# Performance work log

Measured on AMD Instinct MI355X. Metric: run time of the kernel, lower is better.

Reference implementation:

```python
import math
import jax, jax.numpy as jnp
import numpy as np

B, S, E, H = 4, 1024, 1024, 16
DH = E // H
LN_EPS = 1e-5


def _layernorm(x, g, b):
    mu = jnp.mean(x, axis=-1, keepdims=True)
    var = jnp.mean(jnp.square(x - mu), axis=-1, keepdims=True)
    return (x - mu) * jax.lax.rsqrt(var + LN_EPS) * g + b


def _gelu_tanh(x):
    c = math.sqrt(2.0 / math.pi)
    return 0.5 * x * (1.0 + jnp.tanh(c * (x + 0.044715 * x * x * x)))


def setup_inputs() -> dict:
    key = jax.random.key(0)
    ks = jax.random.split(key, 12)
    std = 0.02
    x = jax.random.normal(ks[0], (B, S, E), jnp.float32)
    # additive causal mask: 0 on/below diag, -inf above
    causal_mask = jnp.where(jnp.tril(jnp.ones((S, S), bool)), 0.0, -jnp.inf).astype(jnp.float32)
    inp = dict(
        x=x,
        causal_mask=causal_mask,
        ln1_g=1.0 + std * jax.random.normal(ks[1], (E,), jnp.float32),
        ln1_b=std * jax.random.normal(ks[2], (E,), jnp.float32),
        ln2_g=1.0 + std * jax.random.normal(ks[3], (E,), jnp.float32),
        ln2_b=std * jax.random.normal(ks[4], (E,), jnp.float32),
        w_in=std * jax.random.normal(ks[5], (3 * E, E), jnp.float32),   # packed QKV in_proj_weight
        b_in=jnp.zeros((3 * E,), jnp.float32),
        w_out=std * jax.random.normal(ks[6], (E, E), jnp.float32),      # out_proj.weight
        b_out=jnp.zeros((E,), jnp.float32),
        w_fc=std * jax.random.normal(ks[7], (4 * E, E), jnp.float32),
        b_fc=jnp.zeros((4 * E,), jnp.float32),
        w_proj=std * jax.random.normal(ks[8], (E, 4 * E), jnp.float32),
        b_proj=jnp.zeros((E,), jnp.float32),
    )
    return inp


def reference(x, causal_mask, ln1_g, ln1_b, ln2_g, ln2_b,
              w_in, b_in, w_out, b_out, w_fc, b_fc, w_proj, b_proj):
    # --- attention branch (pre-LN) ---
    h = _layernorm(x, ln1_g, ln1_b)                       # [B,S,E]
    wq, wk, wv = w_in[:E], w_in[E:2 * E], w_in[2 * E:]
    bq, bk, bv = b_in[:E], b_in[E:2 * E], b_in[2 * E:]
    q = (h @ wq.T + bq).reshape(B, S, H, DH)
    k = (h @ wk.T + bk).reshape(B, S, H, DH)
    v = (h @ wv.T + bv).reshape(B, S, H, DH)
    scale = 1.0 / math.sqrt(DH)
    scores = jnp.einsum('bqhd,bkhd->bhqk', q * scale, k) + causal_mask  # [B,H,S,S]
    probs = jax.nn.softmax(scores, axis=-1)
    att = jnp.einsum('bhqk,bkhd->bqhd', probs, v).reshape(B, S, E)
    att = att @ w_out.T + b_out
    att_weights = jnp.mean(probs, axis=1)                 # averaged over heads, [B,S,S]
    x = x + att
    # --- MLP branch (pre-LN) ---
    h2 = _layernorm(x, ln2_g, ln2_b)
    x = x + (_gelu_tanh(h2 @ w_fc.T + b_fc) @ w_proj.T + b_proj)
    return (x, att_weights)
```

## Files before the change

kernel.cpp:

```cpp
#include <hip/hip_runtime.h>

typedef unsigned short u16;
typedef u16   u16x4 __attribute__((ext_vector_type(4)));
typedef u16   u16x8 __attribute__((ext_vector_type(8)));
typedef short s16x8 __attribute__((ext_vector_type(8)));
typedef float f32x4 __attribute__((ext_vector_type(4)));

__device__ __forceinline__ float b2f(u16 u) {
    union { unsigned int i; float f; } v; v.i = ((unsigned int)u) << 16; return v.f;
}
__device__ __forceinline__ u16 f2b(float f) {
    union { float f; unsigned int i; } v; v.f = f;
    unsigned int r = v.i + 0x7fffu + ((v.i >> 16) & 1u);
    return (u16)(r >> 16);
}
__device__ __forceinline__ float gelu_f(float x) {
    float z = 0.7978845608028654f * (x + 0.044715f * x * x * x);
    float e = __expf(2.0f * z);
    float t = 1.0f - 2.0f / (e + 1.0f);
    return 0.5f * x * (1.0f + t);
}
__device__ __forceinline__ void async16(const u16* g, u16* l) {
    __builtin_amdgcn_global_load_lds(
        (const __attribute__((address_space(1))) unsigned int*)g,
        (__attribute__((address_space(3))) unsigned int*)l,
        16, 0, 0);
}

__global__ __launch_bounds__(256)
void detect_k(const u16* __restrict__ x, int* __restrict__ flag)
{
    int gid = blockIdx.x * 256 + threadIdx.x;
    const u16x8 u = *(const u16x8*)(x + (long)gid * 8);
    int bad = 0;
    #pragma unroll
    for (int e = 0; e < 8; e++) {
        int ex = (u[e] >> 7) & 0xFF;
        if (ex >= 187) bad = 1;
    }
    unsigned long long m = __ballot(bad != 0);
    if ((threadIdx.x & 63) == 0 && m != 0ull) atomicOr(flag, 1);
}

__global__ __launch_bounds__(256)
void conv_w_k(const void* __restrict__ s0, const void* __restrict__ s1,
              const void* __restrict__ s2, const void* __restrict__ s3,
              u16* __restrict__ dst, const int* __restrict__ flag)
{
    const long MEG = 1L << 20;
    long gid = ((long)blockIdx.x * 256 + threadIdx.x) * 4;
    const void* s; long off;
    if      (gid <  3*MEG) { s = s0; off = gid; }
    else if (gid <  4*MEG) { s = s1; off = gid - 3*MEG; }
    else if (gid <  8*MEG) { s = s2; off = gid - 4*MEG; }
    else                   { s = s3; off = gid - 8*MEG; }
    u16x4 o;
    if (*flag) {
        const float4 f = *(const float4*)((const float*)s + off);
        o[0] = f2b(f.x); o[1] = f2b(f.y); o[2] = f2b(f.z); o[3] = f2b(f.w);
    } else {
        o = *(const u16x4*)((const u16*)s + off);
    }
    *(u16x4*)(dst + gid) = o;
}

__global__ __launch_bounds__(256)
void conv_small_k(const void* s0, const void* s1, const void* s2, const void* s3,
                  const void* s4, const void* s5, const void* s6, const void* s7,
                  u16* __restrict__ dst, const int* __restrict__ flag)
{
    int gid = blockIdx.x * 256 + threadIdx.x;
    int seg, off;
    if      (gid <  4096) { seg = gid >> 10;  off = gid & 1023; }
    else if (gid <  7168) { seg = 4; off = gid - 4096; }
    else if (gid <  8192) { seg = 5; off = gid - 7168; }
    else if (gid < 12288) { seg = 6; off = gid - 8192; }
    else                  { seg = 7; off = gid - 12288; }
    const void* srcs[8] = {s0, s1, s2, s3, s4, s5, s6, s7};
    const void* s = srcs[seg];
    dst[seg * 4096 + off] = (*flag) ? f2b(((const float*)s)[off]) : ((const u16*)s)[off];
}

__global__ __launch_bounds__(256)
void ln1x_k(const void* __restrict__ xraw, const u16* __restrict__ g,
            const u16* __restrict__ b, u16* __restrict__ xc,
            u16* __restrict__ o, const int* __restrict__ flag)
{
    long row = blockIdx.x;
    int tid = threadIdx.x;
    float v0, v1, v2, v3;
    if (*flag) {
        const float4 f = *(const float4*)((const float*)xraw + row * 1024 + tid * 4);
        v0 = b2f(f2b(f.x)); v1 = b2f(f2b(f.y));
        v2 = b2f(f2b(f.z)); v3 = b2f(f2b(f.w));
    } else {
        const u16x4 u = *(const u16x4*)((const u16*)xraw + row * 1024 + tid * 4);
        v0 = b2f(u[0]); v1 = b2f(u[1]); v2 = b2f(u[2]); v3 = b2f(u[3]);
    }
    u16x4 xv; xv[0] = f2b(v0); xv[1] = f2b(v1); xv[2] = f2b(v2); xv[3] = f2b(v3);
    *(u16x4*)(xc + row * 1024 + tid * 4) = xv;
    float s  = v0 + v1 + v2 + v3;
    float sq = v0*v0 + v1*v1 + v2*v2 + v3*v3;
    #pragma unroll
    for (int off = 32; off; off >>= 1) { s += __shfl_xor(s, off); sq += __shfl_xor(sq, off); }
    __shared__ float sm[8];
    int wid = tid >> 6, lane = tid & 63;
    if (lane == 0) { sm[wid] = s; sm[wid + 4] = sq; }
    __syncthreads();
    s  = sm[0] + sm[1] + sm[2] + sm[3];
    sq = sm[4] + sm[5] + sm[6] + sm[7];
    float mean = s * (1.0f / 1024.0f);
    float var  = sq * (1.0f / 1024.0f) - mean * mean;
    float rs   = rsqrtf(var + 1e-5f);
    u16x4 gg = *(const u16x4*)(g + tid * 4);
    u16x4 bb = *(const u16x4*)(b + tid * 4);
    u16x4 ov;
    ov[0] = f2b((v0 - mean) * rs * b2f(gg[0]) + b2f(bb[0]));
    ov[1] = f2b((v1 - mean) * rs * b2f(gg[1]) + b2f(bb[1]));
    ov[2] = f2b((v2 - mean) * rs * b2f(gg[2]) + b2f(bb[2]));
    ov[3] = f2b((v3 - mean) * rs * b2f(gg[3]) + b2f(bb[3]));
    *(u16x4*)(o + row * 1024 + tid * 4) = ov;
}

__global__ __launch_bounds__(256)
void ln_k(const u16* __restrict__ x, const u16* __restrict__ g,
          const u16* __restrict__ b, u16* __restrict__ o)
{
    long row = blockIdx.x;
    int tid = threadIdx.x;
    const u16x4 u = *(const u16x4*)(x + row * 1024 + tid * 4);
    float v0 = b2f(u[0]), v1 = b2f(u[1]), v2 = b2f(u[2]), v3 = b2f(u[3]);
    float s  = v0 + v1 + v2 + v3;
    float sq = v0*v0 + v1*v1 + v2*v2 + v3*v3;
    #pragma unroll
    for (int off = 32; off; off >>= 1) { s += __shfl_xor(s, off); sq += __shfl_xor(sq, off); }
    __shared__ float sm[8];
    int wid = tid >> 6, lane = tid & 63;
    if (lane == 0) { sm[wid] = s; sm[wid + 4] = sq; }
    __syncthreads();
    s  = sm[0] + sm[1] + sm[2] + sm[3];
    sq = sm[4] + sm[5] + sm[6] + sm[7];
    float mean = s * (1.0f / 1024.0f);
    float var  = sq * (1.0f / 1024.0f) - mean * mean;
    float rs   = rsqrtf(var + 1e-5f);
    u16x4 gg = *(const u16x4*)(g + tid * 4);
    u16x4 bb = *(const u16x4*)(b + tid * 4);
    u16x4 ov;
    ov[0] = f2b((v0 - mean) * rs * b2f(gg[0]) + b2f(bb[0]));
    ov[1] = f2b((v1 - mean) * rs * b2f(gg[1]) + b2f(bb[1]));
    ov[2] = f2b((v2 - mean) * rs * b2f(gg[2]) + b2f(bb[2]));
    ov[3] = f2b((v3 - mean) * rs * b2f(gg[3]) + b2f(bb[3]));
    *(u16x4*)(o + row * 1024 + tid * 4) = ov;
}

__global__ __launch_bounds__(256)
void redln_k(const float* __restrict__ P, long slice,
             const u16* __restrict__ bias, u16* __restrict__ res,
             const u16* __restrict__ g, const u16* __restrict__ b,
             u16* __restrict__ o)
{
    long row = blockIdx.x;
    int tid = threadIdx.x;
    long i = row * 1024 + tid * 4;
    float4 v  = *(const float4*)(P + i);
    float4 p1 = *(const float4*)(P + slice + i);
    u16x4 bb = *(const u16x4*)(bias + tid * 4);
    u16x4 rr = *(const u16x4*)(res + i);
    float v0 = b2f(f2b(v.x + p1.x + b2f(bb[0]) + b2f(rr[0])));
    float v1 = b2f(f2b(v.y + p1.y + b2f(bb[1]) + b2f(rr[1])));
    float v2 = b2f(f2b(v.z + p1.z + b2f(bb[2]) + b2f(rr[2])));
    float v3 = b2f(f2b(v.w + p1.w + b2f(bb[3]) + b2f(rr[3])));
    u16x4 xv; xv[0] = f2b(v0); xv[1] = f2b(v1); xv[2] = f2b(v2); xv[3] = f2b(v3);
    *(u16x4*)(res + i) = xv;
    float s  = v0 + v1 + v2 + v3;
    float sq = v0*v0 + v1*v1 + v2*v2 + v3*v3;
    #pragma unroll
    for (int off = 32; off; off >>= 1) { s += __shfl_xor(s, off); sq += __shfl_xor(sq, off); }
    __shared__ float sm[8];
    int wid = tid >> 6, lane = tid & 63;
    if (lane == 0) { sm[wid] = s; sm[wid + 4] = sq; }
    __syncthreads();
    s  = sm[0] + sm[1] + sm[2] + sm[3];
    sq = sm[4] + sm[5] + sm[6] + sm[7];
    float mean = s * (1.0f / 1024.0f);
    float var  = sq * (1.0f / 1024.0f) - mean * mean;
    float rs   = rsqrtf(var + 1e-5f);
    u16x4 gg = *(const u16x4*)(g + tid * 4);
    u16x4 b2 = *(const u16x4*)(b + tid * 4);
    u16x4 ov;
    ov[0] = f2b((v0 - mean) * rs * b2f(gg[0]) + b2f(b2[0]));
    ov[1] = f2b((v1 - mean) * rs * b2f(gg[1]) + b2f(b2[1]));
    ov[2] = f2b((v2 - mean) * rs * b2f(gg[2]) + b2f(b2[2]));
    ov[3] = f2b((v3 - mean) * rs * b2f(gg[3]) + b2f(b2[3]));
    *(u16x4*)(o + row * 1024 + tid * 4) = ov;
}

__global__ __launch_bounds__(1024)
void smmean_k(u16* __restrict__ probs, void* __restrict__ ow, long ofs,
              const int* __restrict__ flag)
{
    const long MEG = 1L << 20;
    __shared__ float red[16 * 1024];
    int bl = blockIdx.x >> 10;
    int q  = blockIdx.x & 1023;
    int w = threadIdx.x >> 6, lane = threadIdx.x & 63;
    int tile_end = ((q >> 7) + 1) << 7;
    u16* row = probs + (((long)(bl * 16 + w)) << 20) + (long)q * 1024;
    float v[16];
    float m = -3.0e38f;
    #pragma unroll
    for (int c = 0; c < 2; c++) {
        int kb = (c * 64 + lane) * 8;
        if (kb <= q) {
            u16x8 u = *(const u16x8*)(row + kb);
            #pragma unroll
            for (int e = 0; e < 8; e++) {
                if (kb + e <= q) {
                    float f = b2f(u[e]);
                    v[c * 8 + e] = f;
                    m = fmaxf(m, f);
                } else v[c * 8 + e] = -3.0e38f;
            }
        } else {
            #pragma unroll
            for (int e = 0; e < 8; e++) v[c * 8 + e] = -3.0e38f;
        }
    }
    #pragma unroll
    for (int off = 32; off; off >>= 1) m = fmaxf(m, __shfl_xor(m, off));
    float s = 0.0f;
    #pragma unroll
    for (int t = 0; t < 16; t++) {
        float e = (v[t] > -1.0e38f) ? __expf(v[t] - m) : 0.0f;
        v[t] = e; s += e;
    }
    #pragma unroll
    for (int off = 32; off; off >>= 1) s += __shfl_xor(s, off);
    float inv = 1.0f / s;
    #pragma unroll
    for (int c = 0; c < 2; c++) {
        int kb = (c * 64 + lane) * 8;
        float p[8];
        #pragma unroll
        for (int e = 0; e < 8; e++) p[e] = v[c * 8 + e] * inv;
        #pragma unroll
        for (int e = 0; e < 8; e++) red[w * 1024 + kb + e] = p[e];
        if (kb < tile_end) {
            u16x8 o;
            #pragma unroll
            for (int e = 0; e < 8; e++) o[e] = f2b(p[e]);
            *(u16x8*)(row + kb) = o;
        }
    }
    __syncthreads();
    int t = threadIdx.x;
    float acc = 0.0f;
    #pragma unroll
    for (int h = 0; h < 16; h++) acc += red[h * 1024 + t];
    acc *= 0.0625f;
    long idx = ofs + (long)bl * MEG + (long)q * 1024 + t;
    if (*flag) ((float*)ow)[idx] = acc;
    else       ((u16*)ow)[idx]   = f2b(acc);
}

__global__ __launch_bounds__(256)
void reduce_out_k(const float* __restrict__ P, long slice,
                  const u16* __restrict__ bias, const u16* __restrict__ res,
                  void* __restrict__ out, const int* __restrict__ flag)
{
    long i = ((long)blockIdx.x * 256 + threadIdx.x) * 4;
    int gn = (int)(i & 1023);
    float4 v = *(const float4*)(P + i);
    #pragma unroll
    for (int s = 1; s < 4; s++) {
        const float4 p = *(const float4*)(P + (long)s * slice + i);
        v.x += p.x; v.y += p.y; v.z += p.z; v.w += p.w;
    }
    u16x4 bb = *(const u16x4*)(bias + gn);
    u16x4 rr = *(const u16x4*)(res + i);
    v.x += b2f(bb[0]) + b2f(rr[0]);
    v.y += b2f(bb[1]) + b2f(rr[1]);
    v.z += b2f(bb[2]) + b2f(rr[2]);
    v.w += b2f(bb[3]) + b2f(rr[3]);
    if (*flag) {
        *(float4*)((float*)out + i) = v;
    } else {
        u16x4 o;
        o[0] = f2b(v.x); o[1] = f2b(v.y); o[2] = f2b(v.z); o[3] = f2b(v.w);
        *(u16x4*)((u16*)out + i) = o;
    }
}

template<int BN, int EPI>
__global__ __launch_bounds__(256)
void gemm_bt(const u16* __restrict__ A, const u16* __restrict__ Bt,
             u16* __restrict__ C, const u16* __restrict__ bias,
             const u16* __restrict__ res,
             u16* __restrict__ qb, u16* __restrict__ kb, u16* __restrict__ vb,
             int M, int N, int K, int lda, int ldb, int ldc,
             long sA, long sB, long sC,
             const int* __restrict__ oflag, void* __restrict__ oout)
{
    constexpr int BM = 128, BK = 32;
    constexpr int WROWS = (BN == 128) ? 2 : 4;
    constexpr int WCOLS = (BN == 128) ? 2 : 1;
    constexpr int WM = BM / WROWS, WN = BN / WCOLS;
    constexpr int MI = WM / 16, NJ = WN / 16;
    constexpr int BCH = BN * BK / 8 / 256;
    constexpr int SHSZ = 2 * BM * BK + 2 * BN * BK;

    __shared__ alignas(16) u16 shmem[SHSZ];
    u16* AshB = shmem;
    u16* BshB = shmem + 2 * BM * BK;
    u16* Csh  = shmem;

    const int tid = threadIdx.x;
    int tn = blockIdx.x, tm = blockIdx.y;
    const int bz = blockIdx.z;
    if (EPI == 4 && tn > tm) return;

    if (EPI == 1 || EPI == 2 || EPI == 3 || EPI == 6 || EPI == 7) {
        int L = blockIdx.y * gridDim.x + blockIdx.x;
        int xcd = L & 7, idx = L >> 3;
        tn = idx % gridDim.x;
        tm = (idx / gridDim.x) * 8 + xcd;
    }

    const u16* Ab = A + (long)bz * sA;
    const u16* Bb = Bt + (long)bz * sB;

    const int m0 = tm * BM, n0 = tn * BN;
    const int kEff = (EPI == 5) ? (((tm + 1) * BM < K) ? (tm + 1) * BM : K) : K;

    const int w = tid >> 6, lane = tid & 63;
    const int wrow = w % WROWS, wcol = w / WROWS;
    const int mw = wrow * WM, nw = wcol * WN;
    const int lr = lane & 15, quad = lane >> 4;

    const int ca0 = tid, ca1 = 256 + tid;
    const int cb1 = 256 + tid;

    const int ar0 = ca0 >> 2, ac0 = (((ca0 & 3) ^ ((ca0 >> 3) & 3))) * 8;
    const int ar1 = ca1 >> 2, ac1 = (((ca1 & 3) ^ ((ca1 >> 3) & 3))) * 8;
    const int br0 = tid >> 2, bc0 = (((tid & 3) ^ ((tid >> 3) & 3))) * 8;
    const int br1 = cb1 >> 2, bc1 = (((cb1 & 3) ^ ((cb1 >> 3) & 3))) * 8;

    auto stage = [&](int buf, int k0) {
        async16(Ab + (long)(m0 + ar0) * lda + k0 + ac0, &AshB[buf * BM * BK + ca0 * 8]);
        async16(Ab + (long)(m0 + ar1) * lda + k0 + ac1, &AshB[buf * BM * BK + ca1 * 8]);
        async16(Bb + (long)(n0 + br0) * ldb + k0 + bc0, &BshB[buf * BN * BK + tid * 8]);
        if (BCH == 2)
            async16(Bb + (long)(n0 + br1) * ldb + k0 + bc1, &BshB[buf * BN * BK + cb1 * 8]);
    };

    f32x4 acc[MI][NJ] = {};

    const int foff = (quad ^ ((lr >> 1) & 3)) * 8;

    stage(0, 0);
    int cur = 0;
    for (int k0 = 0; k0 < kEff; k0 += BK) {
        __syncthreads();
        if (k0 + BK < kEff) stage(cur ^ 1, k0 + BK);

        s16x8 af[MI], bfr[NJ];
        #pragma unroll
        for (int i = 0; i < MI; i++)
            af[i] = *(const s16x8*)&AshB[cur * BM * BK + (mw + i * 16 + lr) * BK + foff];
        #pragma unroll
        for (int j = 0; j < NJ; j++)
            bfr[j] = *(const s16x8*)&BshB[cur * BN * BK + (nw + j * 16 + lr) * BK + foff];
        #pragma unroll
        for (int i = 0; i < MI; i++)
            #pragma unroll
            for (int j = 0; j < NJ; j++)
                acc[i][j] = __builtin_amdgcn_mfma_f32_16x16x32_bf16(af[i], bfr[j], acc[i][j], 0, 0, 0);
        cur ^= 1;
    }

    if (EPI == 1) {
        const int sel = n0 >> 10;
        const int b = m0 >> 10, sbase = m0 & 1023;
        if (sel < 2) {
            u16* dst = (sel == 0) ? qb : kb;
            #pragma unroll
            for (int i = 0; i < MI; i++)
                #pragma unroll
                for (int j = 0; j < NJ; j++)
                    #pragma unroll
                    for (int r = 0; r < 4; r++) {
                        int gm = m0 + mw + i * 16 + quad * 4 + r;
                        int gn = n0 + nw + j * 16 + lr;
                        float v = acc[i][j][r] + b2f(bias[gn]);
                        int s = gm & 1023, nn = gn & 1023, hh = nn >> 6, d = nn & 63;
                        dst[(((long)(b * 16 + hh) * 1024 + s) << 6) + d] = f2b(v);
                    }
        } else {
            __syncthreads();
            #pragma unroll
            for (int i = 0; i < MI; i++)
                #pragma unroll
                for (int j = 0; j < NJ; j++)
                    #pragma unroll
                    for (int r = 0; r < 4; r++) {
                        int nl = nw + j * 16 + lr;
                        int ml = mw + i * 16 + quad * 4 + r;
                        float v = acc[i][j][r] + b2f(bias[n0 + nl]);
                        Csh[nl * 128 + (((ml >> 3) ^ (nl & 15)) << 3) + (ml & 7)] = f2b(v);
                    }
            __syncthreads();
            const int nv0 = n0 - 2048;
            #pragma unroll
            for (int rep = 0; rep < 8; rep++) {
                int dd = rep * 16 + (tid >> 4);
                int sl = (tid & 15) * 8;
                int dg = nv0 + dd, hh = dg >> 6, dcol = dg & 63;
                u16x8 val = *(const u16x8*)&Csh[dd * 128 + ((((sl >> 3)) ^ (dd & 15)) << 3)];
                *(u16x8*)&vb[(((long)(b * 16 + hh) * 64 + dcol) << 10) + sbase + sl] = val;
            }
        }
        return;
    }

    u16* Cb;
    if (EPI == 5) Cb = C + (long)(bz >> 4) * (1 << 20) + (bz & 15) * 64;
    else          Cb = C + (long)bz * sC;

    #pragma unroll
    for (int i = 0; i < MI; i++) {
        #pragma unroll
        for (int j = 0; j < NJ; j++) {
            #pragma unroll
            for (int r = 0; r < 4; r++) {
                int gm = m0 + mw + i * 16 + quad * 4 + r;
                int gn = n0 + nw + j * 16 + lr;
                float v = acc[i][j][r];
                if (EPI == 5) {
                    Cb[(long)gm * ldc + gn] = f2b(v);
                } else if (EPI == 2) {
                    v += b2f(bias[gn]) + b2f(res[(long)gm * ldc + gn]);
                    Cb[(long)gm * ldc + gn] = f2b(v);
                } else if (EPI == 3) {
                    Cb[(long)gm * ldc + gn] = f2b(gelu_f(v + b2f(bias[gn])));
                } else if (EPI == 4) {
                    if (gn <= gm) Cb[(long)gm * ldc + gn] = f2b(v * 0.125f);
                } else if (EPI == 6) {
                    v += b2f(bias[gn]) + b2f(res[(long)gm * ldc + gn]);
                    long idx = (long)gm * ldc + gn;
                    if (*oflag) ((float*)oout)[idx] = v;
                    else        ((u16*)oout)[idx]   = f2b(v);
                } else if (EPI == 7) {
                    ((float*)oout)[(long)bz * sC + (long)gm * ldc + gn] = v;
                }
            }
        }
    }
}

extern "C" void kernel_launch(void* const* d_in, const int* in_sizes, int n_in,
                              void* d_out, int out_size, void* d_ws, size_t ws_size,
                              hipStream_t stream)
{
    const long MEG = 1L << 20;
    const long KI  = 1024;

    u16* ws = (u16*)d_ws;
    u16* xc    = ws;
    u16* winC  = ws + 4  * MEG;
    u16* woutC = ws + 7  * MEG;
    u16* wfcC  = ws + 8  * MEG;
    u16* wprjC = ws + 12 * MEG;
    u16* sm    = ws + 16 * MEG;
    u16* ln1g = sm + 0*4*KI, *ln1b = sm + 1*4*KI;
    u16* ln2g = sm + 2*4*KI, *ln2b = sm + 3*4*KI;
    u16* binC = sm + 4*4*KI;
    u16* boutC= sm + 5*4*KI;
    u16* bfcC = sm + 6*4*KI;
    u16* bprjC= sm + 7*4*KI;
    int* flag = (int*)(sm + 8*4*KI);
    u16* slotA = ws + 16 * MEG + 64 * KI;
    u16* qB    = slotA + 4  * MEG;
    u16* kB    = slotA + 8  * MEG;
    u16* vT    = slotA + 12 * MEG;
    u16* probs = slotA + 16 * MEG;
    float* part = (float*)(probs + 16 * MEG);

    const long fixed_elems = 32 * MEG + 64 * KI;
    const long avail = (long)(ws_size / 2);
    int chunk = 1;
    if      (avail >= fixed_elems + 64 * MEG) chunk = 4;
    else if (avail >= fixed_elems + 32 * MEG) chunk = 2;
    const bool splitk = (chunk == 4);

    hipMemsetAsync((void*)flag, 0, sizeof(int), stream);
    detect_k<<<32, 256, 0, stream>>>((const u16*)d_in[0], flag);
    conv_w_k<<<12288, 256, 0, stream>>>(d_in[6], d_in[8], d_in[10], d_in[12],
                                        winC, flag);
    conv_small_k<<<52, 256, 0, stream>>>(d_in[2], d_in[3], d_in[4], d_in[5],
                                         d_in[7], d_in[9], d_in[11], d_in[13],
                                         sm, flag);

    u16* h   = slotA;
    u16* att = slotA;
    u16* h2  = slotA;
    u16* act = probs;

    ln1x_k<<<4096, 256, 0, stream>>>(d_in[0], ln1g, ln1b, xc, h, flag);
    gemm_bt<128, 1><<<dim3(24, 32, 1), 256, 0, stream>>>(
        h, winC, nullptr, binC, nullptr, qB, kB, vT,
        4096, 3072, 1024, 1024, 1024, 0, 0, 0, 0, nullptr, nullptr);
    for (int b0 = 0; b0 < 4; b0 += chunk) {
        gemm_bt<128, 4><<<dim3(8, 8, 16 * chunk), 256, 0, stream>>>(
            qB + b0 * MEG, kB + b0 * MEG, probs, nullptr, nullptr,
            nullptr, nullptr, nullptr,
            1024, 1024, 64, 64, 64, 1024, 65536, 65536, 1048576, nullptr, nullptr);
        smmean_k<<<1024 * chunk, 1024, 0, stream>>>(probs, d_out,
                                                    4 * MEG + b0 * MEG, flag);
        gemm_bt<64, 5><<<dim3(1, 8, 16 * chunk), 256, 0, stream>>>(
            probs, vT + b0 * MEG, att + b0 * MEG, nullptr, nullptr,
            nullptr, nullptr, nullptr,
            1024, 64, 1024, 1024, 1024, 1024, 1048576, 65536, 0, nullptr, nullptr);
    }
    if (splitk) {
        gemm_bt<128, 7><<<dim3(8, 32, 2), 256, 0, stream>>>(
            att, woutC, nullptr, nullptr, nullptr, nullptr, nullptr, nullptr,
            4096, 1024, 512, 1024, 1024, 1024, 512, 512, 4 * MEG, nullptr, part);
        redln_k<<<4096, 256, 0, stream>>>(part, 4 * MEG, boutC, xc, ln2g, ln2b, h2);
    } else {
        gemm_bt<128, 2><<<dim3(8, 32, 1), 256, 0, stream>>>(
            att, woutC, xc, boutC, xc, nullptr, nullptr, nullptr,
            4096, 1024, 1024, 1024, 1024, 1024, 0, 0, 0, nullptr, nullptr);
        ln_k<<<4096, 256, 0, stream>>>(xc, ln2g, ln2b, h2);
    }
    gemm_bt<128, 3><<<dim3(32, 32, 1), 256, 0, stream>>>(
        h2, wfcC, act, bfcC, nullptr, nullptr, nullptr, nullptr,
        4096, 4096, 1024, 1024, 1024, 4096, 0, 0, 0, nullptr, nullptr);
    if (splitk) {
        gemm_bt<128, 7><<<dim3(8, 32, 4), 256, 0, stream>>>(
            act, wprjC, nullptr, nullptr, nullptr, nullptr, nullptr, nullptr,
            4096, 1024, 1024, 4096, 4096, 1024, 1024, 1024, 4 * MEG, nullptr, part);
        reduce_out_k<<<4096, 256, 0, stream>>>(part, 4 * MEG, bprjC, xc, d_out, flag);
    } else {
        gemm_bt<128, 6><<<dim3(8, 32, 1), 256, 0, stream>>>(
            act, wprjC, nullptr, bprjC, xc, nullptr, nullptr, nullptr,
            4096, 1024, 4096, 4096, 4096, 1024, 0, 0, 0, flag, d_out);
    }
}
```

Measured before the change: 423.6 us.

## Add 256x256-tile 8-wave pipelined GEMM for MLP fc and proj layers

Adds a new GEMM kernel with 256x256 output tiles, 512 threads and double-buffered async global-to-LDS loads. It uses XOR-swizzled LDS, explicit waitcnt and barrier scheduling, setprio around MFMA bursts, and an XCD-aware block remap. The kernel replaces the 128-tile GEMMs for the MLP fc (with GELU epilogue) and the split-K projection layers, aiming for higher arithmetic intensity and better overlap of loads with MFMA. The hand-tuned waitcnt counts and the missing bounds checks tie it to K being a multiple of 128 and to dimensions divisible by 256.

```diff
diff --git a/kernel.cpp b/kernel.cpp
--- a/kernel.cpp
+++ b/kernel.cpp
@@ -26,6 +26,11 @@
         (__attribute__((address_space(3))) unsigned int*)l,
         16, 0, 0);
 }
+
+#define FEN() asm volatile("" ::: "memory")
+#define BARR() { FEN(); __builtin_amdgcn_s_barrier(); FEN(); }
+#define LGKM0() { asm volatile("s_waitcnt lgkmcnt(0)" ::: "memory"); __builtin_amdgcn_sched_barrier(0); }
+#define VMC(N) asm volatile("s_waitcnt vmcnt(" #N ")" ::: "memory")
 
 __global__ __launch_bounds__(256)
 void detect_k(const u16* __restrict__ x, int* __restrict__ flag)
@@ -289,6 +294,172 @@
         o[0] = f2b(v.x); o[1] = f2b(v.y); o[2] = f2b(v.z); o[3] = f2b(v.w);
         *(u16x4*)((u16*)out + i) = o;
     }
+}
+
+template<int EPI>
+__global__ __launch_bounds__(512, 2)
+void g8(const u16* __restrict__ A, const u16* __restrict__ Bt,
+        u16* __restrict__ C, const u16* __restrict__ bias,
+        float* __restrict__ Cf,
+        int K, int lda, int ldb, int ldc,
+        long sA, long sB, long sC)
+{
+    __shared__ alignas(16) u16 shA[2 * 16384];
+    __shared__ alignas(16) u16 shB[2 * 16384];
+
+    const int tid = threadIdx.x;
+    int tn = blockIdx.x, tm = blockIdx.y;
+    const int bz = blockIdx.z;
+    {
+        int L = blockIdx.y * gridDim.x + blockIdx.x;
+        int xcd = L & 7, idx = L >> 3;
+        tn = idx % gridDim.x;
+        tm = (idx / gridDim.x) * 8 + xcd;
+    }
+    const u16* Ab = A + (long)bz * sA;
+    const u16* Bb = Bt + (long)bz * sB;
+    const int m0 = tm * 256, n0 = tn * 256;
+    const int NT = K >> 6;
+
+    const int w = tid >> 6, lane = tid & 63;
+    const int lr = lane & 15, quad = lane >> 4, sw = lane & 7;
+    const int wm16 = (w >> 2) * 16, wn16 = (w & 3) * 16;
+
+    auto stageH = [&](int tile, int isB, int half) {
+        const u16* src = isB ? Bb : Ab;
+        const int ld = isB ? ldb : lda;
+        const int r0 = (isB ? n0 : m0) + half * 128;
+        u16* dbase = (isB ? shB : shA) + (tile & 1) * 16384 + half * 8192;
+        const long kk = (long)tile << 6;
+        #pragma unroll
+        for (int L2 = 0; L2 < 2; L2++) {
+            int c = L2 * 512 + tid;
+            int rl = c >> 3, sl = c & 7;
+            int kc = sl ^ (rl & 7);
+            async16(src + (long)(r0 + rl) * ld + kk + kc * 8, dbase + c * 8);
+        }
+    };
+
+    f32x4 acc[2][4][2][2] = {};
+    s16x8 aF[4][2], b0F[2][2], b1F[2][2];
+
+    auto rdA = [&](int buf, int ih) {
+        #pragma unroll
+        for (int q = 0; q < 4; q++)
+            #pragma unroll
+            for (int ks = 0; ks < 2; ks++)
+                aF[q][ks] = *(const s16x8*)&shA[buf * 16384 + ih * 8192
+                    + (q * 32 + wm16 + lr) * 64 + ((ks * 4 + quad) ^ sw) * 8];
+    };
+    auto rdB = [&](s16x8 (&bF)[2][2], int buf, int jh) {
+        #pragma unroll
+        for (int r = 0; r < 2; r++)
+            #pragma unroll
+            for (int ks = 0; ks < 2; ks++)
+                bF[r][ks] = *(const s16x8*)&shB[buf * 16384 + jh * 8192
+                    + (r * 64 + wn16 + lr) * 64 + ((ks * 4 + quad) ^ sw) * 8];
+    };
+
+#define MM(IH, JH, BF) do { \
+    __builtin_amdgcn_s_setprio(1); \
+    _Pragma("unroll") \
+    for (int q = 0; q < 4; q++) \
+        _Pragma("unroll") \
+        for (int r = 0; r < 2; r++) \
+            _Pragma("unroll") \
+            for (int ks = 0; ks < 2; ks++) \
+                acc[IH][q][JH][r] = __builtin_amdgcn_mfma_f32_16x16x32_bf16( \
+                    aF[q][ks], BF[r][ks], acc[IH][q][JH][r], 0, 0, 0); \
+    __builtin_amdgcn_s_setprio(0); \
+} while (0)
+
+    stageH(0, 0, 0); stageH(0, 1, 0); stageH(0, 0, 1); stageH(0, 1, 1);
+    stageH(1, 0, 0); stageH(1, 1, 0);
+    VMC(8); BARR();
+
+    for (int it = 0; it < NT - 2; it += 2) {
+        rdA(0, 0); rdB(b0F, 0, 0); stageH(it + 1, 0, 1);
+        BARR(); LGKM0(); MM(0, 0, b0F);
+        FEN(); VMC(6); BARR();
+
+        rdB(b1F, 0, 1); stageH(it + 1, 1, 1);
+        BARR(); LGKM0(); MM(0, 1, b1F);
+        BARR();
+
+        rdA(0, 1); stageH(it + 2, 0, 0);
+        BARR(); LGKM0(); MM(1, 0, b0F);
+        BARR();
+
+        stageH(it + 2, 1, 0);
+        BARR(); LGKM0(); MM(1, 1, b1F);
+        FEN(); VMC(8); BARR();
+
+        rdA(1, 0); rdB(b0F, 1, 0); stageH(it + 2, 0, 1);
+        BARR(); LGKM0(); MM(0, 0, b0F);
+        FEN(); VMC(6); BARR();
+
+        rdB(b1F, 1, 1); stageH(it + 2, 1, 1);
+        BARR(); LGKM0(); MM(0, 1, b1F);
+        BARR();
+
+        rdA(1, 1); stageH(it + 3, 0, 0);
+        BARR(); LGKM0(); MM(1, 0, b0F);
+        BARR();
+
+        stageH(it + 3, 1, 0);
+        BARR(); LGKM0(); MM(1, 1, b1F);
+        FEN(); VMC(8); BARR();
+    }
+
+    rdA(0, 0); rdB(b0F, 0, 0); stageH(NT - 1, 0, 1);
+    BARR(); LGKM0(); MM(0, 0, b0F);
+    FEN(); VMC(6); BARR();
+
+    rdB(b1F, 0, 1); stageH(NT - 1, 1, 1);
+    BARR(); LGKM0(); MM(0, 1, b1F);
+    BARR();
+
+    rdA(0, 1);
+    BARR(); LGKM0(); MM(1, 0, b0F);
+    BARR();
+
+    BARR(); LGKM0(); MM(1, 1, b1F);
+    FEN(); VMC(0); BARR();
+
+    rdA(1, 0); rdB(b0F, 1, 0);
+    BARR(); LGKM0(); MM(0, 0, b0F);
+    BARR();
+
+    rdB(b1F, 1, 1);
+    BARR(); LGKM0(); MM(0, 1, b1F);
+    BARR();
+
+    rdA(1, 1);
+    BARR(); LGKM0(); MM(1, 0, b0F);
+    BARR();
+
+    LGKM0(); MM(1, 1, b1F);
+#undef MM
+
+    #pragma unroll
+    for (int ih = 0; ih < 2; ih++)
+        #pragma unroll
+        for (int q = 0; q < 4; q++)
+            #pragma unroll
+            for (int jh = 0; jh < 2; jh++)
+                #pragma unroll
+                for (int r = 0; r < 2; r++)
+                    #pragma unroll
+                    for (int rr = 0; rr < 4; rr++) {
+                        int gm = m0 + ih * 128 + q * 32 + wm16 + quad * 4 + rr;
+                        int gn = n0 + jh * 128 + r * 64 + wn16 + lr;
+                        float v = acc[ih][q][jh][r][rr];
+                        if (EPI == 3) {
+                            C[(long)gm * ldc + gn] = f2b(gelu_f(v + b2f(bias[gn])));
+                        } else {
+                            Cf[(long)bz * sC + (long)gm * ldc + gn] = v;
+                        }
+                    }
 }
 
 template<int BN, int EPI>
@@ -532,13 +703,13 @@
             4096, 1024, 1024, 1024, 1024, 1024, 0, 0, 0, nullptr, nullptr);
         ln_k<<<4096, 256, 0, stream>>>(xc, ln2g, ln2b, h2);
     }
-    gemm_bt<128, 3><<<dim3(32, 32, 1), 256, 0, stream>>>(
-        h2, wfcC, act, bfcC, nullptr, nullptr, nullptr, nullptr,
-        4096, 4096, 1024, 1024, 1024, 4096, 0, 0, 0, nullptr, nullptr);
+    g8<3><<<dim3(16, 16, 1), 512, 0, stream>>>(
+        h2, wfcC, act, bfcC, nullptr,
+        1024, 1024, 1024, 4096, 0, 0, 0);
     if (splitk) {
-        gemm_bt<128, 7><<<dim3(8, 32, 4), 256, 0, stream>>>(
-            act, wprjC, nullptr, nullptr, nullptr, nullptr, nullptr, nullptr,
-            4096, 1024, 1024, 4096, 4096, 1024, 1024, 1024, 4 * MEG, nullptr, part);
+        g8<7><<<dim3(4, 16, 4), 512, 0, stream>>>(
+            act, wprjC, nullptr, nullptr, part,
+            1024, 4096, 4096, 1024, 1024, 1024, 4 * MEG);
         reduce_out_k<<<4096, 256, 0, stream>>>(part, 4 * MEG, bprjC, xc, d_out, flag);
     } else {
         gemm_bt<128, 6><<<dim3(8, 32, 1), 256, 0, stream>>>(
```

After: 416.6 us. No clear change (-1.6%).
